# Kernel optimization log

Hardware: AMD Instinct MI355X
Metric: run time of the kernel (lower is better)

## Reference

```python
import jax, jax.numpy as jnp
import numpy as np
import jax.lax as lax

EPS = 1e-5

def conv3x3(x, w):
    # x: [B,C,H,W], w: [O,C,3,3], stride 1, padding 1
    return lax.conv_general_dilated(x, w, (1, 1), ((1, 1), (1, 1)),
                                    dimension_numbers=('NCHW', 'OIHW', 'NCHW'))

def bn(x, s, b, m, v):
    inv = s / jnp.sqrt(v + EPS)
    return x * inv[None, :, None, None] + (b - m * inv)[None, :, None, None]

def conv_bn_relu(x, w, s, b, m, v):
    return jax.nn.relu(bn(conv3x3(x, w), s, b, m, v))

def spatial_attention(x, q_w, q_b, v_w, v_b, gamma):
    # Self_attention: q_conv used for both q and k (k_conv is dead in source)
    B, C, H, W = x.shape
    N = H * W
    q = (jnp.einsum('bchw,oc->bohw', x, q_w) + q_b[None, :, None, None]).reshape(B, -1, N)  # [B,Cq,N]
    v = (jnp.einsum('bchw,oc->bohw', x, v_w) + v_b[None, :, None, None]).reshape(B, C, N)   # [B,C,N]
    energy = jnp.einsum('bcn,bcm->bnm', q, q)          # [B,N,N]
    attn = jax.nn.softmax(energy, axis=-1)
    out = jnp.einsum('bcm,bnm->bcn', v, attn)          # v @ attn^T
    return gamma[0] * out.reshape(B, C, H, W) + x

def channel_attention(x, gamma):
    B, C, H, W = x.shape
    xf = x.reshape(B, C, -1)                           # [B,C,N]
    energy = jnp.einsum('bcn,bdn->bcd', xf, xf)        # [B,C,C]
    energy_new = jnp.max(energy, axis=-1, keepdims=True) - energy
    attn = jax.nn.softmax(energy_new, axis=-1)
    out = jnp.einsum('bcd,bdn->bcn', attn, xf)
    return gamma[0] * out.reshape(B, C, H, W) + x

def setup_inputs() -> dict:
    key = jax.random.key(0)
    ks = jax.random.split(key, 32)
    B, Cin, H, W = 4, 512, 64, 64
    Ci, Cq, Cout = 128, 16, 19
    f = jax.random.normal
    u = jax.random.uniform
    d = {}
    d['x'] = f(ks[0], (B, Cin, H, W), jnp.float32)
    d['conv5a_w'] = f(ks[1], (Ci, Cin, 3, 3), jnp.float32) * 0.02
    d['bn5a_s'] = u(ks[2], (Ci,), jnp.float32)
    d['bn5a_b'] = f(ks[3], (Ci,), jnp.float32) * 0.1
    d['bn5a_m'] = f(ks[4], (Ci,), jnp.float32) * 0.1
    d['bn5a_v'] = u(ks[5], (Ci,), jnp.float32) + 0.5
    d['conv5c_w'] = f(ks[6], (Ci, Cin, 3, 3), jnp.float32) * 0.02
    d['bn5c_s'] = u(ks[7], (Ci,), jnp.float32)
    d['bn5c_b'] = f(ks[8], (Ci,), jnp.float32) * 0.1
    d['bn5c_m'] = f(ks[9], (Ci,), jnp.float32) * 0.1
    d['bn5c_v'] = u(ks[10], (Ci,), jnp.float32) + 0.5
    d['q_w'] = f(ks[11], (Cq, Ci), jnp.float32) * 0.05
    d['q_b'] = f(ks[12], (Cq,), jnp.float32) * 0.05
    d['v_w'] = f(ks[13], (Ci, Ci), jnp.float32) * 0.05
    d['v_b'] = f(ks[14], (Ci,), jnp.float32) * 0.05
    d['gamma_sa'] = jnp.zeros((1,), jnp.float32)
    d['gamma_sc'] = jnp.zeros((1,), jnp.float32)
    d['conv51_w'] = f(ks[15], (Ci, Ci, 3, 3), jnp.float32) * 0.03
    d['bn51_s'] = u(ks[16], (Ci,), jnp.float32)
    d['bn51_b'] = f(ks[17], (Ci,), jnp.float32) * 0.1
    d['bn51_m'] = f(ks[18], (Ci,), jnp.float32) * 0.1
    d['bn51_v'] = u(ks[19], (Ci,), jnp.float32) + 0.5
    d['conv52_w'] = f(ks[20], (Ci, Ci, 3, 3), jnp.float32) * 0.03
    d['bn52_s'] = u(ks[21], (Ci,), jnp.float32)
    d['bn52_b'] = f(ks[22], (Ci,), jnp.float32) * 0.1
    d['bn52_m'] = f(ks[23], (Ci,), jnp.float32) * 0.1
    d['bn52_v'] = u(ks[24], (Ci,), jnp.float32) + 0.5
    d['conv8_w'] = f(ks[25], (Cout, Ci), jnp.float32) * 0.05
    d['conv8_b'] = f(ks[26], (Cout,), jnp.float32) * 0.05
    return d

def reference(x, conv5a_w, bn5a_s, bn5a_b, bn5a_m, bn5a_v,
              conv5c_w, bn5c_s, bn5c_b, bn5c_m, bn5c_v,
              q_w, q_b, v_w, v_b, gamma_sa, gamma_sc,
              conv51_w, bn51_s, bn51_b, bn51_m, bn51_v,
              conv52_w, bn52_s, bn52_b, bn52_m, bn52_v,
              conv8_w, conv8_b):
    feat1 = conv_bn_relu(x, conv5a_w, bn5a_s, bn5a_b, bn5a_m, bn5a_v)
    sa_feat = spatial_attention(feat1, q_w, q_b, v_w, v_b, gamma_sa)
    sa_conv = conv_bn_relu(sa_feat, conv51_w, bn51_s, bn51_b, bn51_m, bn51_v)
    feat2 = conv_bn_relu(x, conv5c_w, bn5c_s, bn5c_b, bn5c_m, bn5c_v)
    sc_feat = channel_attention(feat2, gamma_sc)
    sc_conv = conv_bn_relu(sc_feat, conv52_w, bn52_s, bn52_b, bn52_m, bn52_v)
    feat_sum = sa_conv + sc_conv
    # conv8 is a 1x1 conv (Dropout2d is identity in eval mode)
    out = jnp.einsum('bchw,oc->bohw', feat_sum, conv8_w) + conv8_b[None, :, None, None]
    return out
```

## Files before the change

### kernel.cpp

```cpp
#include <hip/hip_runtime.h>
#include <math.h>

#define EPS 1e-5f


typedef unsigned int uint;
typedef unsigned short u16;
typedef u16 u16x4 __attribute__((ext_vector_type(4)));
typedef u16 u16x8 __attribute__((ext_vector_type(8)));
typedef __bf16 bf16x8 __attribute__((ext_vector_type(8)));
typedef float f32x4 __attribute__((ext_vector_type(4)));
typedef float f32x16 __attribute__((ext_vector_type(16)));

__device__ __forceinline__ u16 f2bf(float f) {
    uint u = __float_as_uint(f);
    u = u + 0x7FFF + ((u >> 16) & 1);
    return (u16)(u >> 16);
}
__device__ __forceinline__ float bf2f(u16 h) {
    return __uint_as_float(((uint)h) << 16);
}

__device__ __forceinline__ void gl_lds16(const void* g, void* l) {
    __builtin_amdgcn_global_load_lds(
        (const __attribute__((address_space(1))) unsigned int*)g,
        (__attribute__((address_space(3))) unsigned int*)l, 16, 0, 0);
}

__global__ void bn_prep_all(const float* s0, const float* b0, const float* m0, const float* v0,
                            const float* s1, const float* b1, const float* m1, const float* v1,
                            const float* s2, const float* b2, const float* m2, const float* v2,
                            const float* s3, const float* b3, const float* m3, const float* v3,
                            float* c0, float* c1, float* c2, float* c3) {
    int k = blockIdx.x, i = threadIdx.x;
    const float *s, *bb, *mm, *vv; float* cf;
    if (k == 0)      { s = s0; bb = b0; mm = m0; vv = v0; cf = c0; }
    else if (k == 1) { s = s1; bb = b1; mm = m1; vv = v1; cf = c1; }
    else if (k == 2) { s = s2; bb = b2; mm = m2; vv = v2; cf = c2; }
    else             { s = s3; bb = b3; mm = m3; vv = v3; cf = c3; }
    float inv = s[i] / sqrtf(vv[i] + EPS);
    cf[i] = inv;
    cf[128 + i] = bb[i] - mm[i] * inv;
}

__global__ void border_zero(u16* x0h, u16* x0l, u16* x1h, u16* x1l, u16* x2h, u16* x2l) {
    int p = blockIdx.x;
    int img = p / 260, pe = p % 260;
    int y, x;
    if (pe < 66)       { y = 0;  x = pe; }
    else if (pe < 132) { y = 65; x = pe - 66; }
    else { int q = pe - 132; y = 1 + (q >> 1); x = (q & 1) * 65; }
    int buf = blockIdx.y, tid = threadIdx.x;
    if (buf == 0) {
        size_t base = (((size_t)img * 66 + y) * 66 + x) * 512;
        for (int c = tid; c < 512; c += 256) { x0h[base + c] = 0; x0l[base + c] = 0; }
    } else {
        u16* hh = (buf == 1) ? x1h : x2h;
        u16* ll = (buf == 1) ? x1l : x2l;
        size_t base = (((size_t)img * 66 + y) * 66 + x) * 128;
        for (int c = tid; c < 128; c += 256) { hh[base + c] = 0; ll[base + c] = 0; }
    }
}

template <int CIN>
__global__ void pack_w(const float* __restrict__ w0, u16* __restrict__ h0, u16* __restrict__ l0,
                       const float* __restrict__ w1, u16* __restrict__ h1, u16* __restrict__ l1) {
    const float* w = blockIdx.z ? w1 : w0;
    u16* hh = blockIdx.z ? h1 : h0;
    u16* ll = blockIdx.z ? l1 : l0;
    int i = blockIdx.x * 256 + threadIdx.x;
    int ic = i & (CIN - 1);
    int rest = i / CIN;
    int oc = rest & 127;
    int tap = rest >> 7;
    float f = w[((size_t)oc * CIN + ic) * 9 + tap];
    u16 h = f2bf(f);
    hh[i] = h;
    ll[i] = f2bf(f - bf2f(h));
}

__global__ void pack_x(const float* __restrict__ x, u16* __restrict__ xh, u16* __restrict__ xl) {
    __shared__ float tile[64][68];
    int cb = blockIdx.x, y = blockIdx.y, b = blockIdx.z, tid = threadIdx.x;
    int cl = tid >> 2, seg = tid & 3;
    const float* src = x + (((size_t)b * 512 + cb * 64 + cl) * 64 + y) * 64 + seg * 16;
#pragma unroll
    for (int j = 0; j < 4; j++)
        *(f32x4*)&tile[cl][seg * 16 + j * 4] = *(const f32x4*)(src + j * 4);
    __syncthreads();
    int pxl = tid >> 2, cg = tid & 3;
    u16x8 h0, h1, l0, l1;
#pragma unroll
    for (int j = 0; j < 8; j++) {
        float v = tile[cg * 16 + j][pxl];
        u16 h = f2bf(v); h0[j] = h; l0[j] = f2bf(v - bf2f(h));
    }
#pragma unroll
    for (int j = 0; j < 8; j++) {
        float v = tile[cg * 16 + 8 + j][pxl];
        u16 h = f2bf(v); h1[j] = h; l1[j] = f2bf(v - bf2f(h));
    }
    size_t dst = (((size_t)b * 66 + y + 1) * 66 + (pxl + 1)) * 512 + cb * 64 + cg * 16;
    *(u16x8*)(xh + dst) = h0;  *(u16x8*)(xh + dst + 8) = h1;
    *(u16x8*)(xl + dst) = l0;  *(u16x8*)(xl + dst + 8) = l1;
}

template <int CIN, bool PACKOUT>
__launch_bounds__(256)
__global__ void conv_mfma(const u16* __restrict__ xh0, const u16* __restrict__ xl0,
                          const u16* __restrict__ xh1, const u16* __restrict__ xl1,
                          const u16* __restrict__ wh0, const u16* __restrict__ wl0,
                          const u16* __restrict__ wh1, const u16* __restrict__ wl1,
                          const float* __restrict__ coef0, const float* __restrict__ coef1,
                          float* __restrict__ fo0, float* __restrict__ fo1,
                          u16* __restrict__ ph0, u16* __restrict__ pl0,
                          u16* __restrict__ ph1, u16* __restrict__ pl1) {
    constexpr int ICC = CIN / 32;
    constexpr int NT  = 9 * ICC;
    const int z = blockIdx.z;
    const u16* xh = z ? xh1 : xh0;  const u16* xl = z ? xl1 : xl0;
    const u16* wh = z ? wh1 : wh0;  const u16* wl = z ? wl1 : wl0;
    const float* coef = z ? coef1 : coef0;
    float* fo = z ? fo1 : fo0;
    u16* ph = z ? ph1 : ph0;  u16* pl = z ? pl1 : pl0;

    const int tile = blockIdx.x;
    const int b  = tile >> 5;
    const int y0 = (tile & 31) * 2;
    const int tid = threadIdx.x;

    __shared__ char smem[65536];

    const int cidx = tid & 127;
    const int khv  = (tid >> 7) & 1;
    const u16* bAh = wh + (size_t)cidx * CIN + khv * 8;
    const u16* bAl = wl + (size_t)cidx * CIN + khv * 8;
    const int rr = cidx >> 6, xxc = cidx & 63;
    const size_t rowoff = ((size_t)(b * 66 + y0 + rr) * 66 + xxc) * CIN + khv * 8;
    const u16* bBh = xh + rowoff;
    const u16* bBl = xl + rowoff;
    char* ldst = smem + (tid & 192) * 16;

    const int wid = tid >> 6, lane = tid & 63;
    const int wr = wid >> 1, wc = wid & 1;
    const int l31 = lane & 31, lhi = lane >> 5;
    const int laneA = (lhi * 128 + wr * 64 + l31) * 16;
    const int laneB = 16384 + (lhi * 128 + wc * 64 + l31) * 16;

    f32x16 acc[2][2];
#pragma unroll
    for (int m = 0; m < 2; m++)
#pragma unroll
        for (int n = 0; n < 2; n++)
#pragma unroll
            for (int r = 0; r < 16; r++) acc[m][n][r] = 0.0f;

    auto stage = [&](int t, int db) {
        const int tap = t / ICC;
        const int ic0 = (t % ICC) * 32;
        const int offA = tap * 128 * CIN + ic0;
        const int offB = ((tap / 3) * 66 + (tap % 3)) * CIN + ic0;
        char* ld = ldst + db * 32768;
        gl_lds16(bAh + offA,      ld);
        gl_lds16(bAh + offA + 16, ld + 4096);
        gl_lds16(bAl + offA,      ld + 8192);
        gl_lds16(bAl + offA + 16, ld + 12288);
        gl_lds16(bBh + offB,      ld + 16384);
        gl_lds16(bBh + offB + 16, ld + 20480);
        gl_lds16(bBl + offB,      ld + 24576);
        gl_lds16(bBl + offB + 16, ld + 28672);
    };

    stage(0, 0);
    __syncthreads();

    for (int t = 0; t < NT; ++t) {
        const int db = t & 1;
        if (t + 1 < NT) stage(t + 1, db ^ 1);
        const char* sb = smem + db * 32768;

        bf16x8 Ah[2][2], Al[2][2], Bh[2][2], Bl[2][2];
#pragma unroll
        for (int kk = 0; kk < 2; kk++)
#pragma unroll
            for (int m = 0; m < 2; m++) {
                Ah[m][kk] = *(const bf16x8*)(sb + laneA + kk * 4096 + m * 512);
                Al[m][kk] = *(const bf16x8*)(sb + 8192 + laneA + kk * 4096 + m * 512);
            }
#pragma unroll
        for (int kk = 0; kk < 2; kk++)
#pragma unroll
            for (int n = 0; n < 2; n++) {
                Bh[n][kk] = *(const bf16x8*)(sb + laneB + kk * 4096 + n * 512);
                Bl[n][kk] = *(const bf16x8*)(sb + 8192 + laneB + kk * 4096 + n * 512);
            }
#pragma unroll
        for (int m = 0; m < 2; m++)
#pragma unroll
            for (int n = 0; n < 2; n++)
#pragma unroll
                for (int kk = 0; kk < 2; kk++) {
                    acc[m][n] = __builtin_amdgcn_mfma_f32_32x32x16_bf16(Ah[m][kk], Bh[n][kk], acc[m][n], 0, 0, 0);
                    acc[m][n] = __builtin_amdgcn_mfma_f32_32x32x16_bf16(Ah[m][kk], Bl[n][kk], acc[m][n], 0, 0, 0);
                    acc[m][n] = __builtin_amdgcn_mfma_f32_32x32x16_bf16(Al[m][kk], Bh[n][kk], acc[m][n], 0, 0, 0);
                }
        __syncthreads();
    }

#pragma unroll
    for (int n = 0; n < 2; n++) {
        const int pxl = wc * 64 + n * 32 + l31;
        const int pxg = tile * 128 + pxl;
        const int bb = pxg >> 12, yy = (pxg >> 6) & 63, xg = pxg & 63;
        const size_t fbase = (size_t)pxg * 128;
        const size_t pbase = (((size_t)bb * 66 + yy + 1) * 66 + (xg + 1)) * 128;
#pragma unroll
        for (int m = 0; m < 2; m++)
#pragma unroll
            for (int q = 0; q < 4; q++) {
                const int oc4 = wr * 64 + m * 32 + q * 8 + lhi * 4;
                f32x4 sc = *(const f32x4*)&coef[oc4];
                f32x4 sh = *(const f32x4*)&coef[128 + oc4];
                f32x4 outv;
                u16x4 hv, lv;
#pragma unroll
                for (int j = 0; j < 4; j++) {
                    float v = acc[m][n][q * 4 + j] * sc[j] + sh[j];
                    v = v > 0.0f ? v : 0.0f;
                    outv[j] = v;
                    if (PACKOUT) {
                        u16 h = f2bf(v);
                        hv[j] = h;
                        lv[j] = f2bf(v - bf2f(h));
                    }
                }
                *(f32x4*)&fo[fbase + oc4] = outv;
                if (PACKOUT) {
                    *(u16x4*)&ph[pbase + oc4] = hv;
                    *(u16x4*)&pl[pbase + oc4] = lv;
                }
            }
    }
}

__launch_bounds__(256)
__global__ void conv1x1(const float* __restrict__ fa, const float* __restrict__ fb,
                        const float* __restrict__ w8, const float* __restrict__ b8,
                        float* __restrict__ out) {
    __shared__ float s_w[128 * 20];
    int tid = threadIdx.x;
    for (int i = tid; i < 19 * 128; i += 256) {
        int o = i >> 7, c = i & 127;
        s_w[c * 20 + o] = w8[i];
    }
    __syncthreads();
    size_t px = (size_t)blockIdx.x * 256 + tid;
    const f32x4* A = (const f32x4*)(fa + px * 128);
    const f32x4* B = (const f32x4*)(fb + px * 128);
    float acc[19];
#pragma unroll
    for (int o = 0; o < 19; o++) acc[o] = 0.0f;
    for (int cq = 0; cq < 32; cq++) {
        f32x4 v = A[cq] + B[cq];
#pragma unroll
        for (int j = 0; j < 4; j++) {
            float iv = v[j];
            int c = cq * 4 + j;
#pragma unroll
            for (int o = 0; o < 19; o++) acc[o] += iv * s_w[c * 20 + o];
        }
    }
    int b = px >> 12, n = px & 4095;
#pragma unroll
    for (int o = 0; o < 19; o++)
        out[((size_t)b * 19 + o) * 4096 + n] = acc[o] + b8[o];
}


__global__ void lin_q(const float* __restrict__ g, const float* __restrict__ feat,
                      const float* __restrict__ qw, const float* __restrict__ qb,
                      float* __restrict__ outq) {
    if (g[0] == 0.0f) return;
    __shared__ float s_w[16 * 128];
    int tid = threadIdx.x;
    for (int i = tid; i < 2048; i += 256) s_w[i] = qw[i];
    __syncthreads();
    size_t px = (size_t)blockIdx.x * 256 + tid;
    const float* in = feat + px * 128;
    float acc[16];
#pragma unroll
    for (int o = 0; o < 16; o++) acc[o] = 0.0f;
    for (int c = 0; c < 128; c++) {
        float iv = in[c];
#pragma unroll
        for (int o = 0; o < 16; o++) acc[o] += iv * s_w[o * 128 + c];
    }
#pragma unroll
    for (int o = 0; o < 16; o++) outq[px * 16 + o] = acc[o] + qb[o];
}

__global__ void lin_v(const float* __restrict__ g, const float* __restrict__ feat,
                      const float* __restrict__ vw, const float* __restrict__ vb,
                      float* __restrict__ outv) {
    if (g[0] == 0.0f) return;
    int tid = threadIdx.x;
    size_t px = (size_t)blockIdx.x * 64 + (tid >> 2);
    int q4 = tid & 3;
    const float* in = feat + px * 128;
    float acc[32];
#pragma unroll
    for (int j = 0; j < 32; j++) acc[j] = 0.0f;
    for (int c = 0; c < 128; c++) {
        float iv = in[c];
        for (int j = 0; j < 32; j++) acc[j] += iv * vw[(size_t)(q4 * 32 + j) * 128 + c];
    }
    for (int j = 0; j < 32; j++)
        outv[px * 128 + q4 * 32 + j] = acc[j] + vb[q4 * 32 + j];
}

__global__ void sa_attn(const float* __restrict__ g, const float* __restrict__ qb,
                        const float* __restrict__ vb, const float* __restrict__ feat1,
                        u16* __restrict__ ph, u16* __restrict__ pl) {
    if (g[0] == 0.0f) return;
    float gamma = g[0];
    int b = blockIdx.y, grp = blockIdx.x, tid = threadIdx.x;
    __shared__ float s_e[4096];
    __shared__ float s_red[256];
    __shared__ float s_q[16];
    __shared__ float s_o[256];
    for (int ni = 0; ni < 32; ni++) {
        int n = grp * 32 + ni;
        if (tid < 16) s_q[tid] = qb[((size_t)b * 4096 + n) * 16 + tid];
        __syncthreads();
        float lmax = -1e30f;
        for (int m = tid; m < 4096; m += 256) {
            const float* qm = qb + ((size_t)b * 4096 + m) * 16;
            float e = 0.0f;
#pragma unroll
            for (int k = 0; k < 16; k++) e += s_q[k] * qm[k];
            s_e[m] = e;
            lmax = fmaxf(lmax, e);
        }
        s_red[tid] = lmax;
        __syncthreads();
        for (int s = 128; s > 0; s >>= 1) {
            if (tid < s) s_red[tid] = fmaxf(s_red[tid], s_red[tid + s]);
            __syncthreads();
        }
        float mx = s_red[0];
        __syncthreads();
        float lsum = 0.0f;
        for (int m = tid; m < 4096; m += 256) {
            float p = expf(s_e[m] - mx);
            s_e[m] = p;
            lsum += p;
        }
        s_red[tid] = lsum;
        __syncthreads();
        for (int s = 128; s > 0; s >>= 1) {
            if (tid < s) s_red[tid] += s_red[tid + s];
            __syncthreads();
        }
        float denom = s_red[0];
        __syncthreads();
        int c = tid & 127, half = tid >> 7;
        float acc = 0.0f;
        for (int m = half * 2048; m < half * 2048 + 2048; m++)
            acc += s_e[m] * vb[((size_t)b * 4096 + m) * 128 + c];
        s_o[tid] = acc;
        __syncthreads();
        if (tid < 128) {
            float o = (s_o[tid] + s_o[tid + 128]) / denom;
            float val = feat1[((size_t)b * 4096 + n) * 128 + tid] + gamma * o;
            int yy = n >> 6, xx = n & 63;
            size_t pidx = (((size_t)b * 66 + yy + 1) * 66 + (xx + 1)) * 128 + tid;
            u16 h = f2bf(val);
            ph[pidx] = h;
            pl[pidx] = f2bf(val - bf2f(h));
        }
        __syncthreads();
    }
}

__global__ void ca_attn(const float* __restrict__ g, const float* __restrict__ feat2,
                        u16* __restrict__ ph, u16* __restrict__ pl) {
    if (g[0] == 0.0f) return;
    float gamma = g[0];
    int b = blockIdx.y, crow = blockIdx.x, d = threadIdx.x;
    __shared__ float s_red[128];
    __shared__ float s_attn[128];
    const float* base = feat2 + (size_t)b * 4096 * 128;
    float e = 0.0f;
    for (int n = 0; n < 4096; n++) e += base[(size_t)n * 128 + crow] * base[(size_t)n * 128 + d];
    s_red[d] = e;
    __syncthreads();
    for (int s = 64; s > 0; s >>= 1) {
        if (d < s) s_red[d] = fmaxf(s_red[d], s_red[d + s]);
        __syncthreads();
    }
    float m1 = s_red[0];
    __syncthreads();
    float en = m1 - e;
    s_red[d] = en;
    __syncthreads();
    for (int s = 64; s > 0; s >>= 1) {
        if (d < s) s_red[d] = fmaxf(s_red[d], s_red[d + s]);
        __syncthreads();
    }
    float m2 = s_red[0];
    __syncthreads();
    float p = expf(en - m2);
    s_red[d] = p;
    __syncthreads();
    for (int s = 64; s > 0; s >>= 1) {
        if (d < s) s_red[d] += s_red[d + s];
        __syncthreads();
    }
    s_attn[d] = p / s_red[0];
    __syncthreads();
    for (int n = d; n < 4096; n += 128) {
        float acc = 0.0f;
#pragma unroll 8
        for (int dd = 0; dd < 128; dd++) acc += s_attn[dd] * base[(size_t)n * 128 + dd];
        float val = base[(size_t)n * 128 + crow] + gamma * acc;
        int yy = n >> 6, xx = n & 63;
        size_t pidx = (((size_t)b * 66 + yy + 1) * 66 + (xx + 1)) * 128 + crow;
        u16 h = f2bf(val);
        ph[pidx] = h;
        pl[pidx] = f2bf(val - bf2f(h));
    }
}

extern "C" void kernel_launch(void* const* d_in, const int* in_sizes, int n_in,
                              void* d_out, int out_size, void* d_ws, size_t ws_size,
                              hipStream_t stream) {
    const float* x      = (const float*)d_in[0];
    const float* w5a    = (const float*)d_in[1];
    const float* bn5a_s = (const float*)d_in[2];
    const float* bn5a_b = (const float*)d_in[3];
    const float* bn5a_m = (const float*)d_in[4];
    const float* bn5a_v = (const float*)d_in[5];
    const float* w5c    = (const float*)d_in[6];
    const float* bn5c_s = (const float*)d_in[7];
    const float* bn5c_b = (const float*)d_in[8];
    const float* bn5c_m = (const float*)d_in[9];
    const float* bn5c_v = (const float*)d_in[10];
    const float* q_w    = (const float*)d_in[11];
    const float* q_b    = (const float*)d_in[12];
    const float* v_w    = (const float*)d_in[13];
    const float* v_b    = (const float*)d_in[14];
    const float* g_sa   = (const float*)d_in[15];
    const float* g_sc   = (const float*)d_in[16];
    const float* w51    = (const float*)d_in[17];
    const float* bn51_s = (const float*)d_in[18];
    const float* bn51_b = (const float*)d_in[19];
    const float* bn51_m = (const float*)d_in[20];
    const float* bn51_v = (const float*)d_in[21];
    const float* w52    = (const float*)d_in[22];
    const float* bn52_s = (const float*)d_in[23];
    const float* bn52_b = (const float*)d_in[24];
    const float* bn52_m = (const float*)d_in[25];
    const float* bn52_v = (const float*)d_in[26];
    const float* w8     = (const float*)d_in[27];
    const float* b8     = (const float*)d_in[28];
    float* out = (float*)d_out;
    (void)in_sizes; (void)n_in; (void)out_size; (void)ws_size;

    char* W = (char*)d_ws;
    constexpr size_t XP0 = (size_t)4 * 66 * 66 * 512 * 2;
    constexpr size_t XP1 = (size_t)4 * 66 * 66 * 128 * 2;
    constexpr size_t WPA = (size_t)9 * 128 * 512 * 2;
    constexpr size_t WPB = (size_t)9 * 128 * 128 * 2;
    constexpr size_t FT  = (size_t)4 * 4096 * 128 * 4;
    size_t off = 0;
    u16* xp0h = (u16*)(W + off); off += XP0;
    u16* xp0l = (u16*)(W + off); off += XP0;
    u16* xp1h = (u16*)(W + off); off += XP1;
    u16* xp1l = (u16*)(W + off); off += XP1;
    u16* xp2h = (u16*)(W + off); off += XP1;
    u16* xp2l = (u16*)(W + off); off += XP1;
    u16* wp5ah = (u16*)(W + off); off += WPA;
    u16* wp5al = (u16*)(W + off); off += WPA;
    u16* wp5ch = (u16*)(W + off); off += WPA;
    u16* wp5cl = (u16*)(W + off); off += WPA;
    u16* wp51h = (u16*)(W + off); off += WPB;
    u16* wp51l = (u16*)(W + off); off += WPB;
    u16* wp52h = (u16*)(W + off); off += WPB;
    u16* wp52l = (u16*)(W + off); off += WPB;
    float* c5a = (float*)(W + off); off += 1024;
    float* c5c = (float*)(W + off); off += 1024;
    float* c51 = (float*)(W + off); off += 1024;
    float* c52 = (float*)(W + off); off += 1024;
    float* b0  = (float*)(W + off); off += FT;
    float* b1  = (float*)(W + off); off += FT;
    float* b3a = (float*)(W + off); off += FT;
    float* b3b = (float*)(W + off); off += FT;
    float* qbuf = b3a;
    float* vbuf = (float*)((char*)b3a + 1048576);

    border_zero<<<dim3(1040, 3), 256, 0, stream>>>(xp0h, xp0l, xp1h, xp1l, xp2h, xp2l);
    bn_prep_all<<<4, 128, 0, stream>>>(bn5a_s, bn5a_b, bn5a_m, bn5a_v,
                                       bn5c_s, bn5c_b, bn5c_m, bn5c_v,
                                       bn51_s, bn51_b, bn51_m, bn51_v,
                                       bn52_s, bn52_b, bn52_m, bn52_v,
                                       c5a, c5c, c51, c52);
    pack_w<512><<<dim3(2304, 1, 2), 256, 0, stream>>>(w5a, wp5ah, wp5al, w5c, wp5ch, wp5cl);
    pack_w<128><<<dim3(576, 1, 2), 256, 0, stream>>>(w51, wp51h, wp51l, w52, wp52h, wp52l);
    pack_x<<<dim3(8, 64, 4), 256, 0, stream>>>(x, xp0h, xp0l);

    conv_mfma<512, true><<<dim3(128, 1, 2), 256, 0, stream>>>(
        xp0h, xp0l, xp0h, xp0l,
        wp5ah, wp5al, wp5ch, wp5cl,
        c5a, c5c, b0, b1,
        xp1h, xp1l, xp2h, xp2l);

    lin_q<<<64, 256, 0, stream>>>(g_sa, b0, q_w, q_b, qbuf);
    lin_v<<<256, 256, 0, stream>>>(g_sa, b0, v_w, v_b, vbuf);
    sa_attn<<<dim3(128, 4), 256, 0, stream>>>(g_sa, qbuf, vbuf, b0, xp1h, xp1l);
    ca_attn<<<dim3(128, 4), 128, 0, stream>>>(g_sc, b1, xp2h, xp2l);

    conv_mfma<128, false><<<dim3(128, 1, 2), 256, 0, stream>>>(
        xp1h, xp1l, xp2h, xp2l,
        wp51h, wp51l, wp52h, wp52l,
        c51, c52, b3a, b3b,
        nullptr, nullptr, nullptr, nullptr);

    conv1x1<<<64, 256, 0, stream>>>(b3a, b3b, w8, b8, out);
}
```

Before: 413.3 us.

## Load conv MFMA operands directly from global memory instead of LDS staging

Removes the double-buffered LDS staging (global_load_lds plus a block barrier each step) from the implicit-GEMM conv kernel. Each wave now loads its A (weight) and B (activation) bf16 fragments straight from global memory into registers, with the loop unrolled by two. This drops the LDS traffic and barriers, but the weight and activation fragments are no longer shared across waves through LDS, so redundant global/L2 reads rise and load latency is exposed without explicit prefetch.

Result: slower. 542.8 us (+31.3%).

```diff
diff --git a/kernel.cpp b/kernel.cpp
--- a/kernel.cpp
+++ b/kernel.cpp
@@ -19,12 +19,6 @@
 }
 __device__ __forceinline__ float bf2f(u16 h) {
     return __uint_as_float(((uint)h) << 16);
-}
-
-__device__ __forceinline__ void gl_lds16(const void* g, void* l) {
-    __builtin_amdgcn_global_load_lds(
-        (const __attribute__((address_space(1))) unsigned int*)g,
-        (__attribute__((address_space(3))) unsigned int*)l, 16, 0, 0);
 }
 
 __global__ void bn_prep_all(const float* s0, const float* b0, const float* m0, const float* v0,
@@ -107,14 +101,14 @@
 
 template <int CIN, bool PACKOUT>
 __launch_bounds__(256)
-__global__ void conv_mfma(const u16* __restrict__ xh0, const u16* __restrict__ xl0,
-                          const u16* __restrict__ xh1, const u16* __restrict__ xl1,
-                          const u16* __restrict__ wh0, const u16* __restrict__ wl0,
-                          const u16* __restrict__ wh1, const u16* __restrict__ wl1,
-                          const float* __restrict__ coef0, const float* __restrict__ coef1,
-                          float* __restrict__ fo0, float* __restrict__ fo1,
-                          u16* __restrict__ ph0, u16* __restrict__ pl0,
-                          u16* __restrict__ ph1, u16* __restrict__ pl1) {
+__global__ void conv_direct(const u16* __restrict__ xh0, const u16* __restrict__ xl0,
+                            const u16* __restrict__ xh1, const u16* __restrict__ xl1,
+                            const u16* __restrict__ wh0, const u16* __restrict__ wl0,
+                            const u16* __restrict__ wh1, const u16* __restrict__ wl1,
+                            const float* __restrict__ coef0, const float* __restrict__ coef1,
+                            float* __restrict__ fo0, float* __restrict__ fo1,
+                            u16* __restrict__ ph0, u16* __restrict__ pl0,
+                            u16* __restrict__ ph1, u16* __restrict__ pl1) {
     constexpr int ICC = CIN / 32;
     constexpr int NT  = 9 * ICC;
     const int z = blockIdx.z;
@@ -129,23 +123,12 @@
     const int y0 = (tile & 31) * 2;
     const int tid = threadIdx.x;
 
-    __shared__ char smem[65536];
-
-    const int cidx = tid & 127;
-    const int khv  = (tid >> 7) & 1;
-    const u16* bAh = wh + (size_t)cidx * CIN + khv * 8;
-    const u16* bAl = wl + (size_t)cidx * CIN + khv * 8;
-    const int rr = cidx >> 6, xxc = cidx & 63;
-    const size_t rowoff = ((size_t)(b * 66 + y0 + rr) * 66 + xxc) * CIN + khv * 8;
-    const u16* bBh = xh + rowoff;
-    const u16* bBl = xl + rowoff;
-    char* ldst = smem + (tid & 192) * 16;
-
     const int wid = tid >> 6, lane = tid & 63;
     const int wr = wid >> 1, wc = wid & 1;
     const int l31 = lane & 31, lhi = lane >> 5;
-    const int laneA = (lhi * 128 + wr * 64 + l31) * 16;
-    const int laneB = 16384 + (lhi * 128 + wc * 64 + l31) * 16;
+
+    const size_t aBase = (size_t)(wr * 64 + l31) * CIN + lhi * 8;
+    const size_t bBase = ((size_t)(b * 66 + y0 + wc) * 66 + l31) * CIN + lhi * 8;
 
     f32x16 acc[2][2];
 #pragma unroll
@@ -155,44 +138,29 @@
 #pragma unroll
             for (int r = 0; r < 16; r++) acc[m][n][r] = 0.0f;
 
-    auto stage = [&](int t, int db) {
+#pragma unroll 2
+    for (int t = 0; t < NT; ++t) {
         const int tap = t / ICC;
         const int ic0 = (t % ICC) * 32;
-        const int offA = tap * 128 * CIN + ic0;
-        const int offB = ((tap / 3) * 66 + (tap % 3)) * CIN + ic0;
-        char* ld = ldst + db * 32768;
-        gl_lds16(bAh + offA,      ld);
-        gl_lds16(bAh + offA + 16, ld + 4096);
-        gl_lds16(bAl + offA,      ld + 8192);
-        gl_lds16(bAl + offA + 16, ld + 12288);
-        gl_lds16(bBh + offB,      ld + 16384);
-        gl_lds16(bBh + offB + 16, ld + 20480);
-        gl_lds16(bBl + offB,      ld + 24576);
-        gl_lds16(bBl + offB + 16, ld + 28672);
-    };
-
-    stage(0, 0);
-    __syncthreads();
-
-    for (int t = 0; t < NT; ++t) {
-        const int db = t & 1;
-        if (t + 1 < NT) stage(t + 1, db ^ 1);
-        const char* sb = smem + db * 32768;
+        const size_t offA = (size_t)tap * 128 * CIN + ic0;
+        const size_t offB = (size_t)((tap / 3) * 66 + (tap % 3)) * CIN + ic0;
 
         bf16x8 Ah[2][2], Al[2][2], Bh[2][2], Bl[2][2];
 #pragma unroll
-        for (int kk = 0; kk < 2; kk++)
-#pragma unroll
-            for (int m = 0; m < 2; m++) {
-                Ah[m][kk] = *(const bf16x8*)(sb + laneA + kk * 4096 + m * 512);
-                Al[m][kk] = *(const bf16x8*)(sb + 8192 + laneA + kk * 4096 + m * 512);
+        for (int m = 0; m < 2; m++)
+#pragma unroll
+            for (int kk = 0; kk < 2; kk++) {
+                const size_t a = aBase + offA + (size_t)m * 32 * CIN + kk * 16;
+                Ah[m][kk] = *(const bf16x8*)(wh + a);
+                Al[m][kk] = *(const bf16x8*)(wl + a);
             }
 #pragma unroll
-        for (int kk = 0; kk < 2; kk++)
-#pragma unroll
-            for (int n = 0; n < 2; n++) {
-                Bh[n][kk] = *(const bf16x8*)(sb + laneB + kk * 4096 + n * 512);
-                Bl[n][kk] = *(const bf16x8*)(sb + 8192 + laneB + kk * 4096 + n * 512);
+        for (int n = 0; n < 2; n++)
+#pragma unroll
+            for (int kk = 0; kk < 2; kk++) {
+                const size_t a = bBase + offB + (size_t)n * 32 * CIN + kk * 16;
+                Bh[n][kk] = *(const bf16x8*)(xh + a);
+                Bl[n][kk] = *(const bf16x8*)(xl + a);
             }
 #pragma unroll
         for (int m = 0; m < 2; m++)
@@ -204,7 +172,6 @@
                     acc[m][n] = __builtin_amdgcn_mfma_f32_32x32x16_bf16(Ah[m][kk], Bl[n][kk], acc[m][n], 0, 0, 0);
                     acc[m][n] = __builtin_amdgcn_mfma_f32_32x32x16_bf16(Al[m][kk], Bh[n][kk], acc[m][n], 0, 0, 0);
                 }
-        __syncthreads();
     }
 
 #pragma unroll
@@ -508,7 +475,7 @@
     pack_w<128><<<dim3(576, 1, 2), 256, 0, stream>>>(w51, wp51h, wp51l, w52, wp52h, wp52l);
     pack_x<<<dim3(8, 64, 4), 256, 0, stream>>>(x, xp0h, xp0l);
 
-    conv_mfma<512, true><<<dim3(128, 1, 2), 256, 0, stream>>>(
+    conv_direct<512, true><<<dim3(128, 1, 2), 256, 0, stream>>>(
         xp0h, xp0l, xp0h, xp0l,
         wp5ah, wp5al, wp5ch, wp5cl,
         c5a, c5c, b0, b1,
@@ -519,7 +486,7 @@
     sa_attn<<<dim3(128, 4), 256, 0, stream>>>(g_sa, qbuf, vbuf, b0, xp1h, xp1l);
     ca_attn<<<dim3(128, 4), 128, 0, stream>>>(g_sc, b1, xp2h, xp2l);
 
-    conv_mfma<128, false><<<dim3(128, 1, 2), 256, 0, stream>>>(
+    conv_direct<128, false><<<dim3(128, 1, 2), 256, 0, stream>>>(
         xp1h, xp1l, xp2h, xp2l,
         wp51h, wp51l, wp52h, wp52l,
         c51, c52, b3a, b3b,
```

## Triple-buffer conv LDS staging and prefetch register fragments ahead of MFMA

Applied to the files above, without the earlier changes.

Replaces the double-buffered conv main loop with a three-buffer LDS ring. The loop is unrolled by two, with ping-pong register fragment sets, so the next tile's LDS reads and global-to-LDS loads are issued before the current MFMA block runs. Explicit vmcnt waits and raw barriers replace __syncthreads, and s_setprio raises wave priority around the MFMA burst. LDS use grows to 96KB per block, which may reduce occupancy and raises register pressure from the duplicate fragment arrays.

After: 415.6 us. Within noise of the previous version (+0.6%).

```diff
diff --git a/kernel.cpp b/kernel.cpp
--- a/kernel.cpp
+++ b/kernel.cpp
@@ -11,6 +11,10 @@
 typedef __bf16 bf16x8 __attribute__((ext_vector_type(8)));
 typedef float f32x4 __attribute__((ext_vector_type(4)));
 typedef float f32x16 __attribute__((ext_vector_type(16)));
+
+#define WAIT_VM8()  asm volatile("s_waitcnt vmcnt(8)" ::: "memory")
+#define WAIT_VM0()  asm volatile("s_waitcnt vmcnt(0)" ::: "memory")
+#define BARRIER()   asm volatile("s_barrier" ::: "memory")
 
 __device__ __forceinline__ u16 f2bf(float f) {
     uint u = __float_as_uint(f);
@@ -105,6 +109,40 @@
     *(u16x8*)(xl + dst) = l0;  *(u16x8*)(xl + dst + 8) = l1;
 }
 
+#define READ_FRAGS(AH, AL, BH, BL, sbp)                                          \
+    {                                                                            \
+        const char* sb_ = (sbp);                                                 \
+        _Pragma("unroll")                                                        \
+        for (int kk = 0; kk < 2; kk++) {                                         \
+            _Pragma("unroll")                                                    \
+            for (int m = 0; m < 2; m++) {                                        \
+                AH[m][kk] = *(const bf16x8*)(sb_ + laneA + kk * 4096 + m * 512); \
+                AL[m][kk] = *(const bf16x8*)(sb_ + 8192 + laneA + kk * 4096 + m * 512); \
+            }                                                                    \
+            _Pragma("unroll")                                                    \
+            for (int n = 0; n < 2; n++) {                                        \
+                BH[n][kk] = *(const bf16x8*)(sb_ + laneB + kk * 4096 + n * 512); \
+                BL[n][kk] = *(const bf16x8*)(sb_ + 8192 + laneB + kk * 4096 + n * 512); \
+            }                                                                    \
+        }                                                                        \
+    }
+
+#define DO_MFMA(AH, AL, BH, BL)                                                  \
+    {                                                                            \
+        __builtin_amdgcn_s_setprio(1);                                           \
+        _Pragma("unroll")                                                        \
+        for (int m = 0; m < 2; m++)                                              \
+            _Pragma("unroll")                                                    \
+            for (int n = 0; n < 2; n++)                                          \
+                _Pragma("unroll")                                                \
+                for (int kk = 0; kk < 2; kk++) {                                 \
+                    acc[m][n] = __builtin_amdgcn_mfma_f32_32x32x16_bf16(AH[m][kk], BH[n][kk], acc[m][n], 0, 0, 0); \
+                    acc[m][n] = __builtin_amdgcn_mfma_f32_32x32x16_bf16(AH[m][kk], BL[n][kk], acc[m][n], 0, 0, 0); \
+                    acc[m][n] = __builtin_amdgcn_mfma_f32_32x32x16_bf16(AL[m][kk], BH[n][kk], acc[m][n], 0, 0, 0); \
+                }                                                                \
+        __builtin_amdgcn_s_setprio(0);                                           \
+    }
+
 template <int CIN, bool PACKOUT>
 __launch_bounds__(256)
 __global__ void conv_mfma(const u16* __restrict__ xh0, const u16* __restrict__ xl0,
@@ -117,6 +155,7 @@
                           u16* __restrict__ ph1, u16* __restrict__ pl1) {
     constexpr int ICC = CIN / 32;
     constexpr int NT  = 9 * ICC;
+    static_assert(NT % 2 == 0, "NT must be even");
     const int z = blockIdx.z;
     const u16* xh = z ? xh1 : xh0;  const u16* xl = z ? xl1 : xl0;
     const u16* wh = z ? wh1 : wh0;  const u16* wl = z ? wl1 : wl0;
@@ -129,7 +168,7 @@
     const int y0 = (tile & 31) * 2;
     const int tid = threadIdx.x;
 
-    __shared__ char smem[65536];
+    __shared__ char smem[98304];
 
     const int cidx = tid & 127;
     const int khv  = (tid >> 7) & 1;
@@ -155,12 +194,12 @@
 #pragma unroll
             for (int r = 0; r < 16; r++) acc[m][n][r] = 0.0f;
 
-    auto stage = [&](int t, int db) {
+    auto stage = [&](int t, int buf) {
         const int tap = t / ICC;
         const int ic0 = (t % ICC) * 32;
         const int offA = tap * 128 * CIN + ic0;
         const int offB = ((tap / 3) * 66 + (tap % 3)) * CIN + ic0;
-        char* ld = ldst + db * 32768;
+        char* ld = ldst + buf * 32768;
         gl_lds16(bAh + offA,      ld);
         gl_lds16(bAh + offA + 16, ld + 4096);
         gl_lds16(bAl + offA,      ld + 8192);
@@ -172,39 +211,27 @@
     };
 
     stage(0, 0);
-    __syncthreads();
-
-    for (int t = 0; t < NT; ++t) {
-        const int db = t & 1;
-        if (t + 1 < NT) stage(t + 1, db ^ 1);
-        const char* sb = smem + db * 32768;
-
-        bf16x8 Ah[2][2], Al[2][2], Bh[2][2], Bl[2][2];
-#pragma unroll
-        for (int kk = 0; kk < 2; kk++)
-#pragma unroll
-            for (int m = 0; m < 2; m++) {
-                Ah[m][kk] = *(const bf16x8*)(sb + laneA + kk * 4096 + m * 512);
-                Al[m][kk] = *(const bf16x8*)(sb + 8192 + laneA + kk * 4096 + m * 512);
-            }
-#pragma unroll
-        for (int kk = 0; kk < 2; kk++)
-#pragma unroll
-            for (int n = 0; n < 2; n++) {
-                Bh[n][kk] = *(const bf16x8*)(sb + laneB + kk * 4096 + n * 512);
-                Bl[n][kk] = *(const bf16x8*)(sb + 8192 + laneB + kk * 4096 + n * 512);
-            }
-#pragma unroll
-        for (int m = 0; m < 2; m++)
-#pragma unroll
-            for (int n = 0; n < 2; n++)
-#pragma unroll
-                for (int kk = 0; kk < 2; kk++) {
-                    acc[m][n] = __builtin_amdgcn_mfma_f32_32x32x16_bf16(Ah[m][kk], Bh[n][kk], acc[m][n], 0, 0, 0);
-                    acc[m][n] = __builtin_amdgcn_mfma_f32_32x32x16_bf16(Ah[m][kk], Bl[n][kk], acc[m][n], 0, 0, 0);
-                    acc[m][n] = __builtin_amdgcn_mfma_f32_32x32x16_bf16(Al[m][kk], Bh[n][kk], acc[m][n], 0, 0, 0);
-                }
-        __syncthreads();
+    stage(1, 1);
+    WAIT_VM8();
+    BARRIER();
+    bf16x8 A0h[2][2], A0l[2][2], B0h[2][2], B0l[2][2];
+    bf16x8 A1h[2][2], A1l[2][2], B1h[2][2], B1l[2][2];
+    READ_FRAGS(A0h, A0l, B0h, B0l, smem);
+
+    for (int t = 0; t < NT; t += 2) {
+        WAIT_VM0();
+        BARRIER();
+        READ_FRAGS(A1h, A1l, B1h, B1l, smem + ((t + 1) % 3) * 32768);
+        if (t + 2 < NT) stage(t + 2, (t + 2) % 3);
+        DO_MFMA(A0h, A0l, B0h, B0l);
+
+        WAIT_VM0();
+        BARRIER();
+        if (t + 2 < NT) {
+            READ_FRAGS(A0h, A0l, B0h, B0l, smem + ((t + 2) % 3) * 32768);
+            if (t + 3 < NT) stage(t + 3, (t + 3) % 3);
+        }
+        DO_MFMA(A1h, A1l, B1h, B1l);
     }
 
 #pragma unroll
```
